# Kernel tuning notes

Measured on AMD Instinct MI355X. Metric: run time of the kernel, lower is better.

## Reference

```python
import jax, jax.numpy as jnp
import numpy as np

N_NODES = 5000
N_EDGES = 100000
MUL = 64            # env_embed_multiplicity
LATENT = 256        # ScalarMLPFunction latent width
NODE_DIM = 64
RADIAL_DIM = 8
R_MAX = 5.0
P_CUT = 6.0
AVG_NEIGH = 20.0
W_ENV = MUL * 2     # env_weighter weight_numel: mul * n_input_irreps (0e, 1o)
INV_SQRT3 = 1.0 / np.sqrt(3.0)


def _w(k, fi, fo):
    return jax.random.normal(k, (fi, fo), dtype=jnp.float32) / np.sqrt(fi)


def setup_inputs() -> dict:
    key = jax.random.key(0)
    i = iter(jax.random.split(key, 24))
    inp = {}
    inp['node_attrs'] = jax.random.normal(next(i), (N_NODES, NODE_DIM), dtype=jnp.float32)
    inp['edge_radial_attrs'] = jax.random.uniform(next(i), (N_EDGES, RADIAL_DIM), dtype=jnp.float32)
    inp['edge_angular_attrs'] = jax.random.normal(next(i), (N_EDGES, 4), dtype=jnp.float32)
    inp['edge_lengths'] = jax.random.uniform(next(i), (N_EDGES,), dtype=jnp.float32) * R_MAX
    inp['edge_index'] = jax.random.randint(next(i), (2, N_EDGES), 0, N_NODES, dtype=jnp.int32)
    # two-body latent MLP (layer 0): in = 2*node_dim + radial_dim
    inp['tb_w0'] = _w(next(i), 2 * NODE_DIM + RADIAL_DIM, LATENT)
    inp['tb_w1'] = _w(next(i), LATENT, LATENT)
    inp['tb_w2'] = _w(next(i), LATENT, LATENT)
    # latent MLP (layer 1): in = latent + mul * n_scalar_outs(=2)
    inp['lat1_w0'] = _w(next(i), LATENT + 2 * MUL, LATENT)
    inp['lat1_w1'] = _w(next(i), LATENT, LATENT)
    # env_embed MLPs: layer0 emits env weights + per-channel gate + feature-init weights
    inp['env0_w'] = _w(next(i), LATENT, 2 * W_ENV + MUL)
    inp['env1_w'] = _w(next(i), LATENT, W_ENV + MUL)
    # per-irrep env linears (0e block, 1o block)
    inp['envlin0'] = jax.random.normal(next(i), (2, MUL, MUL), dtype=jnp.float32) / np.sqrt(MUL)
    inp['envlin1'] = jax.random.normal(next(i), (2, MUL, MUL), dtype=jnp.float32) / np.sqrt(MUL)
    # post-TP irrep linears: layer0 maps 2 blocks -> 1 block per irrep type
    inp['lin0_sw'] = jax.random.normal(next(i), (2, MUL, MUL), dtype=jnp.float32) / np.sqrt(2 * MUL)
    inp['lin0_vw'] = jax.random.normal(next(i), (2, MUL, MUL), dtype=jnp.float32) / np.sqrt(2 * MUL)
    # last layer keeps full_out_irreps: 2 blocks -> 2 blocks per irrep type
    inp['lin1_sw'] = jax.random.normal(next(i), (2, 2, MUL, MUL), dtype=jnp.float32) / np.sqrt(2 * MUL)
    inp['lin1_vw'] = jax.random.normal(next(i), (2, 2, MUL, MUL), dtype=jnp.float32) / np.sqrt(2 * MUL)
    # final latent: in = latent + mul*2 -> mul*2 scalar gates
    inp['fin_w0'] = _w(next(i), LATENT + 2 * MUL, LATENT)
    inp['fin_w1'] = _w(next(i), LATENT, 2 * MUL)
    inp['res_p'] = jnp.zeros((2,), dtype=jnp.float32)
    return inp


def _poly_cutoff(r):
    x = r / R_MAX
    p = P_CUT
    out = (1.0 - ((p + 1.0) * (p + 2.0) / 2.0) * x ** p
           + p * (p + 2.0) * x ** (p + 1.0)
           - (p * (p + 1.0) / 2.0) * x ** (p + 2.0))
    return jnp.where(x < 1.0, out, 0.0)


def _mlp(x, ws):
    for j, w in enumerate(ws):
        x = x @ w
        if j < len(ws) - 1:
            x = jax.nn.silu(x)
    return x


def _env_weighter(sh, w):
    # sh [E,4] = (0e | 1o), w [E, MUL*2] -> scalar [E,MUL], vector [E,MUL,3]
    w = w.reshape(-1, MUL, 2)
    return w[..., 0] * sh[:, None, 0], w[..., 1:2] * sh[:, None, 1:4]


def _tp_uuu(s1, v1, s2, v2):
    # per-channel (uuu) CG tensor product, instructions:
    #   0e x 0e -> 0e ; 1o x 1o -> 0e ; 0e x 1o -> 1o ; 1o x 0e -> 1o
    ts = jnp.stack([s1 * s2, jnp.sum(v1 * v2, -1) * INV_SQRT3], axis=1)          # [E,2,MUL]
    tv = jnp.stack([s1[..., None] * v2 * INV_SQRT3,
                    v1 * s2[..., None] * INV_SQRT3], axis=1)                      # [E,2,MUL,3]
    return ts, tv


def reference(node_attrs, edge_radial_attrs, edge_angular_attrs, edge_lengths,
              edge_index, tb_w0, tb_w1, tb_w2, lat1_w0, lat1_w1, env0_w, env1_w,
              envlin0, envlin1, lin0_sw, lin0_vw, lin1_sw, lin1_vw,
              fin_w0, fin_w1, res_p):
    center, neigh = edge_index[0], edge_index[1]
    cut = _poly_cutoff(edge_lengths)[:, None]                                     # [E,1]

    # ---- layer 0: two-body latent ----
    x = jnp.concatenate([node_attrs[center], node_attrs[neigh], edge_radial_attrs], -1)
    latents = cut * _mlp(x, [tb_w0, tb_w1, tb_w2])                                # [E,LATENT]

    w_all = latents @ env0_w
    w_env, gate, w_feat = (w_all[:, :W_ENV], w_all[:, W_ENV:W_ENV + MUL],
                           w_all[:, W_ENV + MUL:])
    fs, fv = _env_weighter(edge_angular_attrs, w_feat)                            # [E,MUL],[E,MUL,3]
    fs = fs * gate
    fv = fv * gate[..., None]
    es, ev = _env_weighter(edge_angular_attrs, w_env)
    ns = jax.ops.segment_sum(es, center, num_segments=N_NODES) / AVG_NEIGH        # [N,MUL]
    nv = jax.ops.segment_sum(ev, center, num_segments=N_NODES) / AVG_NEIGH        # [N,MUL,3]
    ns = jnp.einsum('nu,uv->nv', ns, envlin0[0])
    nv = jnp.einsum('nuc,uv->nvc', nv, envlin0[1])
    ts, tv = _tp_uuu(fs, fv, ns[center], nv[center])
    scalars = ts.reshape(-1, 2 * MUL)
    fs = jnp.einsum('eiu,iuv->ev', ts, lin0_sw)                                   # [E,MUL]
    fv = jnp.einsum('eiuc,iuv->evc', tv, lin0_vw)                                 # [E,MUL,3]

    # ---- layer 1: latent resnet + tp ----
    new_lat = _mlp(jnp.concatenate([latents, scalars], -1), [lat1_w0, lat1_w1])
    a = jax.nn.sigmoid(res_p[1])
    latents = jnp.sqrt(1.0 - a) * latents + jnp.sqrt(a) * cut * new_lat

    w_all = latents @ env1_w
    w_env, gate = w_all[:, :W_ENV], w_all[:, W_ENV:]
    fs = fs * gate
    fv = fv * gate[..., None]
    es, ev = _env_weighter(edge_angular_attrs, w_env)
    ns = jax.ops.segment_sum(es, center, num_segments=N_NODES) / AVG_NEIGH
    nv = jax.ops.segment_sum(ev, center, num_segments=N_NODES) / AVG_NEIGH
    ns = jnp.einsum('nu,uv->nv', ns, envlin1[0])
    nv = jnp.einsum('nuc,uv->nvc', nv, envlin1[1])
    ts, tv = _tp_uuu(fs, fv, ns[center], nv[center])
    scalars = ts.reshape(-1, 2 * MUL)
    fs = jnp.einsum('eiu,iouv->eov', ts, lin1_sw)                                 # [E,2,MUL]
    fv = jnp.einsum('eiuc,iouv->eovc', tv, lin1_vw)                               # [E,2,MUL,3]

    # ---- final latent gates the scalar channels, reshape back ----
    fin = _mlp(jnp.concatenate([latents, scalars], -1), [fin_w0, fin_w1])         # [E,2*MUL]
    fs = fs * fin.reshape(-1, 2, MUL)
    return jnp.concatenate([fs.reshape(-1, 2 * MUL), fv.reshape(-1, 2 * MUL * 3)], -1)  # [E,512]
```

## Files before the change

### kernel.cpp

```cpp
#include <hip/hip_runtime.h>
#include <math.h>

typedef unsigned short u16;
typedef unsigned int   u32;

#define E_EDGES 100000
#define NNODES  5000
#define INV_SQRT3 0.57735026918962576f
#define INV_AVG   0.05f

typedef short bf16x8 __attribute__((ext_vector_type(8)));
typedef float f32x4  __attribute__((ext_vector_type(4)));

__device__ __forceinline__ float us2f(u16 u) {
    union { float f; u32 i; } c; c.i = ((u32)u) << 16; return c.f;
}
__device__ __forceinline__ u16 f2us(float f) {
    union { float f; u32 i; } c; c.f = f;
    u32 x = c.i;
    x += 0x7fffu + ((x >> 16) & 1u);
    return (u16)(x >> 16);
}
__device__ __forceinline__ float siluf(float x) { return x / (1.f + expf(-x)); }

__device__ __forceinline__ void gl_lds16(const void* g, void* l) {
    auto* s = (const __attribute__((address_space(1))) void*)g;
    auto* d = (__attribute__((address_space(3))) void*)l;
    __builtin_amdgcn_global_load_lds(s, d, 16, 0, 0);
}

template <int EPI>
__global__ __launch_bounds__(256) void mgemm2_k(
    const u16* __restrict__ X1, int ldx1, int K1,
    const u16* __restrict__ X2, int ldx2, int K2,
    const u16* __restrict__ Wh, const u16* __restrict__ Wl, int ldk,
    u16* __restrict__ Y, int ldy, int M, int N,
    const float* __restrict__ cut, const float* __restrict__ resp,
    const u16* __restrict__ F, float* __restrict__ OUTF)
{
    __shared__ short lA[4096];
    __shared__ short lBh[4096];
    __shared__ short lBl[4096];
    const int lane = threadIdx.x & 63;
    const int w    = threadIdx.x >> 6;
    const int q    = lane >> 4;
    const int r16  = lane & 15;
    const int m0 = blockIdx.x * 128;
    const int n0 = blockIdx.y * 128;
    const int wr0 = (w >> 1) * 64;
    const int wc0 = (w & 1) * 64;
    const int Kt = K1 + K2;

    f32x4 acc[4][4];
#pragma unroll
    for (int i = 0; i < 4; ++i)
#pragma unroll
        for (int j = 0; j < 4; ++j) acc[i][j] = (f32x4){0.f, 0.f, 0.f, 0.f};

    for (int k0 = 0; k0 < Kt; k0 += 32) {
        const u16* xs; int ldx, kb;
        if (k0 < K1) { xs = X1; ldx = ldx1; kb = k0; }
        else         { xs = X2; ldx = ldx2; kb = k0 - K1; }
#pragma unroll
        for (int i = 0; i < 2; ++i) {
            const int j = w * 2 + i;
            int row = m0 + (j & 1) * 64 + lane;
            row = row < M ? row : M - 1;
            gl_lds16(xs + (size_t)row * ldx + kb + (j >> 1) * 8, &lA[j * 512]);
        }
#pragma unroll
        for (int i = 0; i < 2; ++i) {
            const int j = w * 2 + i;
            const size_t wo = (size_t)(n0 + (j & 1) * 64 + lane) * ldk + k0 + (j >> 1) * 8;
            gl_lds16(Wh + wo, &lBh[j * 512]);
            gl_lds16(Wl + wo, &lBl[j * 512]);
        }
        __syncthreads();
        bf16x8 a[4], bh[4], bl[4];
#pragma unroll
        for (int rt = 0; rt < 4; ++rt)
            a[rt] = *(const bf16x8*)&lA[q * 1024 + (wr0 + rt * 16 + r16) * 8];
#pragma unroll
        for (int ct = 0; ct < 4; ++ct) {
            bh[ct] = *(const bf16x8*)&lBh[q * 1024 + (wc0 + ct * 16 + r16) * 8];
            bl[ct] = *(const bf16x8*)&lBl[q * 1024 + (wc0 + ct * 16 + r16) * 8];
        }
#pragma unroll
        for (int rt = 0; rt < 4; ++rt)
#pragma unroll
            for (int ct = 0; ct < 4; ++ct) {
                acc[rt][ct] = __builtin_amdgcn_mfma_f32_16x16x32_bf16(a[rt], bh[ct], acc[rt][ct], 0, 0, 0);
                acc[rt][ct] = __builtin_amdgcn_mfma_f32_16x16x32_bf16(a[rt], bl[ct], acc[rt][ct], 0, 0, 0);
            }
        __syncthreads();
    }
    float c1 = 0.f, c2a = 0.f;
    if (EPI == 3) {
        float aa = 1.f / (1.f + expf(-resp[1]));
        c1 = sqrtf(1.f - aa);
        c2a = sqrtf(aa);
    }
#pragma unroll
    for (int rt = 0; rt < 4; ++rt) {
#pragma unroll
        for (int r = 0; r < 4; ++r) {
            const int row = m0 + wr0 + rt * 16 + q * 4 + r;
            if (row < M) {
                float sc = 1.f;
                if (EPI == 2) sc = cut[row];
                float c2 = 0.f;
                if (EPI == 3) c2 = c2a * cut[row];
                int e3 = 0, cc = 0;
                if (EPI == 5) { e3 = row / 3; cc = row - e3 * 3; }
#pragma unroll
                for (int ct = 0; ct < 4; ++ct) {
                    const int col = n0 + wc0 + ct * 16 + r16;
                    if (col < N) {
                        float v = acc[rt][ct][r];
                        if (EPI == 1) v = siluf(v);
                        if (EPI == 2) v *= sc;
                        if (EPI == 3) v = c1 * us2f(Y[(size_t)row * ldy + col]) + c2 * v;
                        if (EPI == 4) {
                            OUTF[(size_t)row * 512 + col] = v * us2f(F[(size_t)row * 128 + col]);
                        } else if (EPI == 5) {
                            OUTF[(size_t)e3 * 512 + 128 + (col >> 6) * 192 + (col & 63) * 3 + cc] = v;
                        } else {
                            Y[(size_t)row * ldy + col] = f2us(v);
                        }
                    }
                }
            }
        }
    }
}

__global__ __launch_bounds__(128) void mgemm_k(
    const u16* __restrict__ X1, int ldx1, int K1,
    const u16* __restrict__ Wh, const u16* __restrict__ Wl, int ldk,
    u16* __restrict__ Y, int ldy, int M)
{
    __shared__ short lA[4096];
    __shared__ short lBh[2048];
    __shared__ short lBl[2048];
    const int lane = threadIdx.x & 63;
    const int w    = threadIdx.x >> 6;
    const int q    = lane >> 4;
    const int r16  = lane & 15;
    const int m0 = blockIdx.x * 128;
    const int n0 = blockIdx.y * 64;
    const int Kt = K1;

    f32x4 acc[4][4];
#pragma unroll
    for (int i = 0; i < 4; ++i)
#pragma unroll
        for (int j = 0; j < 4; ++j) acc[i][j] = (f32x4){0.f, 0.f, 0.f, 0.f};

    for (int k0 = 0; k0 < Kt; k0 += 32) {
#pragma unroll
        for (int i = 0; i < 4; ++i) {
            const int j = w * 4 + i;
            int row = m0 + (j & 1) * 64 + lane;
            row = row < M ? row : M - 1;
            gl_lds16(X1 + (size_t)row * ldx1 + k0 + (j >> 1) * 8, &lA[j * 512]);
        }
#pragma unroll
        for (int i = 0; i < 2; ++i) {
            const int j = w * 2 + i;
            const size_t wo = (size_t)(n0 + lane) * ldk + k0 + j * 8;
            gl_lds16(Wh + wo, &lBh[j * 512]);
            gl_lds16(Wl + wo, &lBl[j * 512]);
        }
        __syncthreads();
        bf16x8 a[4], bh[4], bl[4];
#pragma unroll
        for (int rt = 0; rt < 4; ++rt)
            a[rt] = *(const bf16x8*)&lA[q * 1024 + (w * 64 + rt * 16 + r16) * 8];
#pragma unroll
        for (int ct = 0; ct < 4; ++ct) {
            bh[ct] = *(const bf16x8*)&lBh[q * 512 + (ct * 16 + r16) * 8];
            bl[ct] = *(const bf16x8*)&lBl[q * 512 + (ct * 16 + r16) * 8];
        }
#pragma unroll
        for (int rt = 0; rt < 4; ++rt)
#pragma unroll
            for (int ct = 0; ct < 4; ++ct) {
                acc[rt][ct] = __builtin_amdgcn_mfma_f32_16x16x32_bf16(a[rt], bh[ct], acc[rt][ct], 0, 0, 0);
                acc[rt][ct] = __builtin_amdgcn_mfma_f32_16x16x32_bf16(a[rt], bl[ct], acc[rt][ct], 0, 0, 0);
            }
        __syncthreads();
    }
#pragma unroll
    for (int rt = 0; rt < 4; ++rt) {
#pragma unroll
        for (int r = 0; r < 4; ++r) {
            const int row = m0 + w * 64 + rt * 16 + q * 4 + r;
            if (row < M) {
#pragma unroll
                for (int ct = 0; ct < 4; ++ct)
                    Y[(size_t)row * ldy + n0 + ct * 16 + r16] = f2us(acc[rt][ct][r]);
            }
        }
    }
}

template <int MODE>
__global__ __launch_bounds__(256) void split_w_k(
    const float* __restrict__ src, u16* __restrict__ hi, u16* __restrict__ lo,
    int Ksrc, int Nsrc, int Kpad, int Npad)
{
    int idx = blockIdx.x * 256 + threadIdx.x;
    if (idx >= Npad * Kpad) return;
    int n = idx / Kpad, k = idx - n * Kpad;
    float wv = 0.f;
    if (k < Ksrc && n < Nsrc) {
        if (MODE == 0) wv = src[(size_t)k * Nsrc + n];
        else           wv = src[(k >> 6) * 8192 + (n >> 6) * 4096 + (k & 63) * 64 + (n & 63)];
    }
    u16 h = f2us(wv);
    hi[idx] = h;
    lo[idx] = f2us(wv - us2f(h));
}

__global__ __launch_bounds__(256) void prep_edges_k(
    const float* __restrict__ na, const float* __restrict__ radial,
    const float* __restrict__ lengths, const int* __restrict__ eidx,
    u16* __restrict__ X0, float* __restrict__ cut)
{
    int idx = blockIdx.x * 256 + threadIdx.x;
    if (idx >= E_EDGES * 160) return;
    int e = idx / 160;
    int k = idx - e * 160;
    float v = 0.f;
    if (k < 64)       v = na[(size_t)eidx[e] * 64 + k];
    else if (k < 128) v = na[(size_t)eidx[E_EDGES + e] * 64 + (k - 64)];
    else if (k < 136) v = radial[(size_t)e * 8 + (k - 128)];
    X0[idx] = f2us(v);
    if (k == 136) {
        float x = lengths[e] * 0.2f;
        float x3 = x * x * x;
        float x6 = x3 * x3, x7 = x6 * x, x8 = x7 * x;
        float o = 1.f - 28.f * x6 + 48.f * x7 - 21.f * x8;
        cut[e] = (x < 1.f) ? o : 0.f;
    }
}

__global__ __launch_bounds__(256) void hist_k(const int* __restrict__ eidx, int* __restrict__ cnt)
{
    int e = blockIdx.x * 256 + threadIdx.x;
    if (e < E_EDGES) atomicAdd(&cnt[eidx[e]], 1);
}

__global__ __launch_bounds__(256) void scan_k(const int* __restrict__ cnt, int* __restrict__ offs)
{
    __shared__ int buf[256];
    __shared__ int base;
    if (threadIdx.x == 0) base = 0;
    __syncthreads();
    for (int start = 0; start < NNODES; start += 256) {
        int i = start + threadIdx.x;
        int v = (i < NNODES) ? cnt[i] : 0;
        buf[threadIdx.x] = v;
        __syncthreads();
        for (int d = 1; d < 256; d <<= 1) {
            int t = (threadIdx.x >= d) ? buf[threadIdx.x - d] : 0;
            __syncthreads();
            buf[threadIdx.x] += t;
            __syncthreads();
        }
        if (i < NNODES) offs[i] = base + buf[threadIdx.x] - v;
        __syncthreads();
        if (threadIdx.x == 255) base += buf[255];
        __syncthreads();
    }
}

__global__ __launch_bounds__(256) void scatter_k(
    const int* __restrict__ eidx, const int* __restrict__ offs,
    int* __restrict__ cur, int* __restrict__ perm)
{
    int e = blockIdx.x * 256 + threadIdx.x;
    if (e >= E_EDGES) return;
    int n = eidx[e];
    int p = atomicAdd(&cur[n], 1);
    perm[offs[n] + p] = e;
}

template <int LD>
__global__ __launch_bounds__(64) void envsum_k(
    const u16* __restrict__ wall, const float* __restrict__ ang,
    const int* __restrict__ perm, const int* __restrict__ offs, const int* __restrict__ cnt,
    const float* __restrict__ envlin,
    float* __restrict__ ns_e, float* __restrict__ nv_e)
{
    const int n = blockIdx.x, lane = threadIdx.x;
    const int s = offs[n], c = cnt[n];
    float a0 = 0.f, a1 = 0.f, a2 = 0.f, a3 = 0.f;
    for (int i = 0; i < c; ++i) {
        int e = perm[s + i];
        u32 pw = *(const u32*)(wall + (size_t)e * LD + 2 * lane);
        float we0 = us2f((u16)(pw & 0xffffu)), we1 = us2f((u16)(pw >> 16));
        float4 sh = *(const float4*)(ang + (size_t)e * 4);
        a0 = fmaf(we0, sh.x, a0);
        a1 = fmaf(we1, sh.y, a1);
        a2 = fmaf(we1, sh.z, a2);
        a3 = fmaf(we1, sh.w, a3);
    }
    __shared__ float ss[64], sv0[64], sv1[64], sv2[64];
    ss[lane] = a0; sv0[lane] = a1; sv1[lane] = a2; sv2[lane] = a3;
    __syncthreads();
    const float* L0 = envlin;
    const float* L1 = envlin + 4096;
    float b0 = 0.f, b1 = 0.f, b2 = 0.f, b3 = 0.f;
#pragma unroll 8
    for (int u = 0; u < 64; ++u) {
        float l0 = L0[u * 64 + lane], l1 = L1[u * 64 + lane];
        b0 = fmaf(ss[u],  l0, b0);
        b1 = fmaf(sv0[u], l1, b1);
        b2 = fmaf(sv1[u], l1, b2);
        b3 = fmaf(sv2[u], l1, b3);
    }
    ns_e[n * 64 + lane]           = b0 * INV_AVG;
    nv_e[n * 192 + lane]          = b1 * INV_AVG;
    nv_e[n * 192 + 64 + lane]     = b2 * INV_AVG;
    nv_e[n * 192 + 128 + lane]    = b3 * INV_AVG;
}

__global__ __launch_bounds__(256) void tp0f_k(
    const u16* __restrict__ wall, const float* __restrict__ ang,
    const float* __restrict__ ns_e, const float* __restrict__ nv_e,
    const int* __restrict__ eidx, u16* __restrict__ ts, u16* __restrict__ tv)
{
    int idx = blockIdx.x * 256 + threadIdx.x;
    if (idx >= E_EDGES * 64) return;
    int e = idx >> 6, u = idx & 63;
    int ce = eidx[e];
    const u16* wr = wall + (size_t)e * 320;
    float g   = us2f(wr[128 + u]);
    u32 pw = *(const u32*)&wr[192 + 2 * u];
    float wf0 = us2f((u16)(pw & 0xffffu)), wf1 = us2f((u16)(pw >> 16));
    float4 sh = *(const float4*)(ang + (size_t)e * 4);
    float f  = wf0 * sh.x * g;
    float b0 = wf1 * sh.y * g;
    float b1 = wf1 * sh.z * g;
    float b2 = wf1 * sh.w * g;
    float ns = ns_e[ce * 64 + u];
    float n0 = nv_e[ce * 192 + u], n1 = nv_e[ce * 192 + 64 + u], n2 = nv_e[ce * 192 + 128 + u];
    ts[(size_t)e * 128 + u]      = f2us(f * ns);
    ts[(size_t)e * 128 + 64 + u] = f2us((b0 * n0 + b1 * n1 + b2 * n2) * INV_SQRT3);
    size_t tb = (size_t)e * 384;
    tv[tb + u]             = f2us(f * n0 * INV_SQRT3);
    tv[tb + 128 + u]       = f2us(f * n1 * INV_SQRT3);
    tv[tb + 256 + u]       = f2us(f * n2 * INV_SQRT3);
    tv[tb + 64 + u]        = f2us(b0 * ns * INV_SQRT3);
    tv[tb + 128 + 64 + u]  = f2us(b1 * ns * INV_SQRT3);
    tv[tb + 256 + 64 + u]  = f2us(b2 * ns * INV_SQRT3);
}

__global__ __launch_bounds__(256) void tp1f_k(
    const u16* __restrict__ fs1, const u16* __restrict__ fv1,
    const u16* __restrict__ wall,
    const float* __restrict__ ns_e, const float* __restrict__ nv_e,
    const int* __restrict__ eidx, u16* __restrict__ ts, u16* __restrict__ tv)
{
    int idx = blockIdx.x * 256 + threadIdx.x;
    if (idx >= E_EDGES * 64) return;
    int e = idx >> 6, u = idx & 63;
    int ce = eidx[e];
    float g = us2f(wall[(size_t)e * 192 + 128 + u]);
    float f  = us2f(fs1[(size_t)e * 64 + u]) * g;
    float b0 = us2f(fv1[((size_t)e * 3 + 0) * 64 + u]) * g;
    float b1 = us2f(fv1[((size_t)e * 3 + 1) * 64 + u]) * g;
    float b2 = us2f(fv1[((size_t)e * 3 + 2) * 64 + u]) * g;
    float ns = ns_e[ce * 64 + u];
    float n0 = nv_e[ce * 192 + u], n1 = nv_e[ce * 192 + 64 + u], n2 = nv_e[ce * 192 + 128 + u];
    ts[(size_t)e * 128 + u]      = f2us(f * ns);
    ts[(size_t)e * 128 + 64 + u] = f2us((b0 * n0 + b1 * n1 + b2 * n2) * INV_SQRT3);
    size_t tb = (size_t)e * 384;
    tv[tb + u]             = f2us(f * n0 * INV_SQRT3);
    tv[tb + 128 + u]       = f2us(f * n1 * INV_SQRT3);
    tv[tb + 256 + u]       = f2us(f * n2 * INV_SQRT3);
    tv[tb + 64 + u]        = f2us(b0 * ns * INV_SQRT3);
    tv[tb + 128 + 64 + u]  = f2us(b1 * ns * INV_SQRT3);
    tv[tb + 256 + 64 + u]  = f2us(b2 * ns * INV_SQRT3);
}

static void mgemm2(hipStream_t s, int epi,
                   const u16* X1, int ldx1, int K1,
                   const u16* X2, int ldx2, int K2,
                   const u16* Wh, const u16* Wl, int ldk,
                   u16* Y, int ldy, int M, int N,
                   const float* cut, const float* resp,
                   const u16* F, float* OUTF)
{
    dim3 grid((M + 127) / 128, (N + 127) / 128);
    dim3 block(256);
    if (epi == 0)      mgemm2_k<0><<<grid, block, 0, s>>>(X1, ldx1, K1, X2, ldx2, K2, Wh, Wl, ldk, Y, ldy, M, N, cut, resp, F, OUTF);
    else if (epi == 1) mgemm2_k<1><<<grid, block, 0, s>>>(X1, ldx1, K1, X2, ldx2, K2, Wh, Wl, ldk, Y, ldy, M, N, cut, resp, F, OUTF);
    else if (epi == 2) mgemm2_k<2><<<grid, block, 0, s>>>(X1, ldx1, K1, X2, ldx2, K2, Wh, Wl, ldk, Y, ldy, M, N, cut, resp, F, OUTF);
    else if (epi == 3) mgemm2_k<3><<<grid, block, 0, s>>>(X1, ldx1, K1, X2, ldx2, K2, Wh, Wl, ldk, Y, ldy, M, N, cut, resp, F, OUTF);
    else if (epi == 4) mgemm2_k<4><<<grid, block, 0, s>>>(X1, ldx1, K1, X2, ldx2, K2, Wh, Wl, ldk, Y, ldy, M, N, cut, resp, F, OUTF);
    else               mgemm2_k<5><<<grid, block, 0, s>>>(X1, ldx1, K1, X2, ldx2, K2, Wh, Wl, ldk, Y, ldy, M, N, cut, resp, F, OUTF);
}

static void split_w(hipStream_t s, int mode, const float* src, u16* hi, u16* lo,
                    int Ksrc, int Nsrc, int Kpad, int Npad)
{
    int n = Npad * Kpad;
    dim3 grid((n + 255) / 256), block(256);
    if (mode == 0) split_w_k<0><<<grid, block, 0, s>>>(src, hi, lo, Ksrc, Nsrc, Kpad, Npad);
    else           split_w_k<1><<<grid, block, 0, s>>>(src, hi, lo, Ksrc, Nsrc, Kpad, Npad);
}

extern "C" void kernel_launch(void* const* d_in, const int* in_sizes, int n_in,
                              void* d_out, int out_size, void* d_ws, size_t ws_size,
                              hipStream_t stream)
{
    const float* node_attrs = (const float*)d_in[0];
    const float* radial     = (const float*)d_in[1];
    const float* ang        = (const float*)d_in[2];
    const float* lengths    = (const float*)d_in[3];
    const int*   eidx       = (const int*)d_in[4];
    const float* tb_w0      = (const float*)d_in[5];
    const float* tb_w1      = (const float*)d_in[6];
    const float* tb_w2      = (const float*)d_in[7];
    const float* lat1_w0    = (const float*)d_in[8];
    const float* lat1_w1    = (const float*)d_in[9];
    const float* env0_w     = (const float*)d_in[10];
    const float* env1_w     = (const float*)d_in[11];
    const float* envlin0    = (const float*)d_in[12];
    const float* envlin1    = (const float*)d_in[13];
    const float* lin0_sw    = (const float*)d_in[14];
    const float* lin0_vw    = (const float*)d_in[15];
    const float* lin1_sw    = (const float*)d_in[16];
    const float* lin1_vw    = (const float*)d_in[17];
    const float* fin_w0     = (const float*)d_in[18];
    const float* fin_w1     = (const float*)d_in[19];
    const float* res_p      = (const float*)d_in[20];

    const size_t E = E_EDGES;
    unsigned char* ws = (unsigned char*)d_ws;
    size_t off = 0;
    auto take = [&](size_t n) -> void* {
        void* p = ws + off;
        off += (n + 255) & ~(size_t)255;
        return p;
    };
    u16*  X0   = (u16*)take(E * 160 * 2);
    float* cut = (float*)take(E * 4);
    u16*  hA   = (u16*)take(E * 256 * 2);
    u16*  hB   = (u16*)take(E * 256 * 2);
    u16*  lat  = (u16*)take(E * 256 * 2);
    u16*  wall = (u16*)take(E * 320 * 2);
    u16*  ts   = (u16*)take(E * 128 * 2);
    u16*  tv   = (u16*)take(E * 384 * 2);
    u16*  fs1  = (u16*)take(E * 64 * 2);
    u16*  fv1  = (u16*)take(E * 192 * 2);
    float* ns_e  = (float*)take((size_t)NNODES * 64 * 4);
    float* nv_e  = (float*)take((size_t)NNODES * 192 * 4);
    float* ns2_e = (float*)take((size_t)NNODES * 64 * 4);
    float* nv2_e = (float*)take((size_t)NNODES * 192 * 4);

    int* cnt  = (int*)take(NNODES * 4);
    int* cur  = (int*)take(NNODES * 4);
    int* offs = (int*)take(NNODES * 4);
    int* perm = (int*)take(E * 4);

    u16* W0h  = (u16*)take(256 * 160 * 2); u16* W0l  = (u16*)take(256 * 160 * 2);
    u16* W1h  = (u16*)take(65536 * 2);     u16* W1l  = (u16*)take(65536 * 2);
    u16* W2h  = (u16*)take(65536 * 2);     u16* W2l  = (u16*)take(65536 * 2);
    u16* We0h = (u16*)take(384 * 256 * 2); u16* We0l = (u16*)take(384 * 256 * 2);
    u16* WL0h = (u16*)take(98304 * 2);     u16* WL0l = (u16*)take(98304 * 2);
    u16* WL1h = (u16*)take(65536 * 2);     u16* WL1l = (u16*)take(65536 * 2);
    u16* We1h = (u16*)take(256 * 256 * 2); u16* We1l = (u16*)take(256 * 256 * 2);
    u16* S0h  = (u16*)take(8192 * 2);      u16* S0l  = (u16*)take(8192 * 2);
    u16* V0h  = (u16*)take(8192 * 2);      u16* V0l  = (u16*)take(8192 * 2);
    u16* S1h  = (u16*)take(16384 * 2);     u16* S1l  = (u16*)take(16384 * 2);
    u16* V1h  = (u16*)take(16384 * 2);     u16* V1l  = (u16*)take(16384 * 2);
    u16* WF0h = (u16*)take(98304 * 2);     u16* WF0l = (u16*)take(98304 * 2);
    u16* WF1h = (u16*)take(32768 * 2);     u16* WF1l = (u16*)take(32768 * 2);

    hipMemsetAsync(cnt, 0, NNODES * 4, stream);
    hipMemsetAsync(cur, 0, NNODES * 4, stream);

    split_w(stream, 0, tb_w0,   W0h,  W0l,  136, 256, 160, 256);
    split_w(stream, 0, tb_w1,   W1h,  W1l,  256, 256, 256, 256);
    split_w(stream, 0, tb_w2,   W2h,  W2l,  256, 256, 256, 256);
    split_w(stream, 0, env0_w,  We0h, We0l, 256, 320, 256, 384);
    split_w(stream, 0, lat1_w0, WL0h, WL0l, 384, 256, 384, 256);
    split_w(stream, 0, lat1_w1, WL1h, WL1l, 256, 256, 256, 256);
    split_w(stream, 0, env1_w,  We1h, We1l, 256, 192, 256, 256);
    split_w(stream, 0, lin0_sw, S0h,  S0l,  128, 64,  128, 64);
    split_w(stream, 0, lin0_vw, V0h,  V0l,  128, 64,  128, 64);
    split_w(stream, 1, lin1_sw, S1h,  S1l,  128, 128, 128, 128);
    split_w(stream, 1, lin1_vw, V1h,  V1l,  128, 128, 128, 128);
    split_w(stream, 0, fin_w0,  WF0h, WF0l, 384, 256, 384, 256);
    split_w(stream, 0, fin_w1,  WF1h, WF1l, 256, 128, 256, 128);

    prep_edges_k<<<(E_EDGES * 160) / 256, 256, 0, stream>>>(node_attrs, radial, lengths, eidx, X0, cut);

    hist_k<<<(E_EDGES + 255) / 256, 256, 0, stream>>>(eidx, cnt);
    scan_k<<<1, 256, 0, stream>>>(cnt, offs);
    scatter_k<<<(E_EDGES + 255) / 256, 256, 0, stream>>>(eidx, offs, cur, perm);

    mgemm2(stream, 1, X0, 160, 160, nullptr, 0, 0, W0h, W0l, 160, hA, 256, E_EDGES, 256, nullptr, nullptr, nullptr, nullptr);
    mgemm2(stream, 1, hA, 256, 256, nullptr, 0, 0, W1h, W1l, 256, hB, 256, E_EDGES, 256, nullptr, nullptr, nullptr, nullptr);
    mgemm2(stream, 2, hB, 256, 256, nullptr, 0, 0, W2h, W2l, 256, lat, 256, E_EDGES, 256, cut, nullptr, nullptr, nullptr);

    mgemm2(stream, 0, lat, 256, 256, nullptr, 0, 0, We0h, We0l, 256, wall, 320, E_EDGES, 320, nullptr, nullptr, nullptr, nullptr);
    envsum_k<320><<<NNODES, 64, 0, stream>>>(wall, ang, perm, offs, cnt, envlin0, ns_e, nv_e);
    tp0f_k<<<(E_EDGES * 64) / 256, 256, 0, stream>>>(wall, ang, ns_e, nv_e, eidx, ts, tv);
    {
        dim3 block(128);
        dim3 g1((E_EDGES + 127) / 128, 1);
        mgemm_k<<<g1, block, 0, stream>>>(ts, 128, 128, S0h, S0l, 128, fs1, 64, E_EDGES);
        dim3 g2((3 * E_EDGES + 127) / 128, 1);
        mgemm_k<<<g2, block, 0, stream>>>(tv, 128, 128, V0h, V0l, 128, fv1, 64, 3 * E_EDGES);
    }

    mgemm2(stream, 1, lat, 256, 256, ts, 128, 128, WL0h, WL0l, 384, hA, 256, E_EDGES, 256, nullptr, nullptr, nullptr, nullptr);
    mgemm2(stream, 3, hA, 256, 256, nullptr, 0, 0, WL1h, WL1l, 256, lat, 256, E_EDGES, 256, cut, res_p, nullptr, nullptr);

    mgemm2(stream, 0, lat, 256, 256, nullptr, 0, 0, We1h, We1l, 256, wall, 192, E_EDGES, 192, nullptr, nullptr, nullptr, nullptr);
    envsum_k<192><<<NNODES, 64, 0, stream>>>(wall, ang, perm, offs, cnt, envlin1, ns2_e, nv2_e);
    tp1f_k<<<(E_EDGES * 64) / 256, 256, 0, stream>>>(fs1, fv1, wall, ns2_e, nv2_e, eidx, ts, tv);

    mgemm2(stream, 1, lat, 256, 256, ts, 128, 128, WF0h, WF0l, 384, hA, 256, E_EDGES, 256, nullptr, nullptr, nullptr, nullptr);
    mgemm2(stream, 0, hA, 256, 256, nullptr, 0, 0, WF1h, WF1l, 256, hB, 128, E_EDGES, 128, nullptr, nullptr, nullptr, nullptr);

    mgemm2(stream, 4, ts, 128, 128, nullptr, 0, 0, S1h, S1l, 128, nullptr, 0, E_EDGES, 128, nullptr, nullptr, hB, (float*)d_out);
    mgemm2(stream, 5, tv, 128, 128, nullptr, 0, 0, V1h, V1l, 128, nullptr, 0, 3 * E_EDGES, 128, nullptr, nullptr, nullptr, (float*)d_out);
}
```

Baseline: 1.311 ms.

## Double-buffer LDS tiles in both MFMA GEMM kernels to overlap loads with compute

Both GEMM kernels now keep two LDS buffers for the A, B-high and B-low tiles. The next K-slice is issued with global_load_lds into the spare buffer before the MFMAs run on the current one, and a single barrier per iteration replaces the old load-barrier-compute-barrier sequence. The aim is to hide global-to-LDS latency behind matrix math. In exchange, LDS use per block doubles, to 48KB in the 256-thread kernel, which can lower the number of resident blocks per CU.

```diff
diff --git a/kernel.cpp b/kernel.cpp
--- a/kernel.cpp
+++ b/kernel.cpp
@@ -38,9 +38,9 @@
     const float* __restrict__ cut, const float* __restrict__ resp,
     const u16* __restrict__ F, float* __restrict__ OUTF)
 {
-    __shared__ short lA[4096];
-    __shared__ short lBh[4096];
-    __shared__ short lBl[4096];
+    __shared__ short lA[2][4096];
+    __shared__ short lBh[2][4096];
+    __shared__ short lBl[2][4096];
     const int lane = threadIdx.x & 63;
     const int w    = threadIdx.x >> 6;
     const int q    = lane >> 4;
@@ -51,13 +51,7 @@
     const int wc0 = (w & 1) * 64;
     const int Kt = K1 + K2;
 
-    f32x4 acc[4][4];
-#pragma unroll
-    for (int i = 0; i < 4; ++i)
-#pragma unroll
-        for (int j = 0; j < 4; ++j) acc[i][j] = (f32x4){0.f, 0.f, 0.f, 0.f};
-
-    for (int k0 = 0; k0 < Kt; k0 += 32) {
+    auto stage = [&](int k0, int buf) {
         const u16* xs; int ldx, kb;
         if (k0 < K1) { xs = X1; ldx = ldx1; kb = k0; }
         else         { xs = X2; ldx = ldx2; kb = k0 - K1; }
@@ -66,24 +60,36 @@
             const int j = w * 2 + i;
             int row = m0 + (j & 1) * 64 + lane;
             row = row < M ? row : M - 1;
-            gl_lds16(xs + (size_t)row * ldx + kb + (j >> 1) * 8, &lA[j * 512]);
+            gl_lds16(xs + (size_t)row * ldx + kb + (j >> 1) * 8, &lA[buf][j * 512]);
         }
 #pragma unroll
         for (int i = 0; i < 2; ++i) {
             const int j = w * 2 + i;
             const size_t wo = (size_t)(n0 + (j & 1) * 64 + lane) * ldk + k0 + (j >> 1) * 8;
-            gl_lds16(Wh + wo, &lBh[j * 512]);
-            gl_lds16(Wl + wo, &lBl[j * 512]);
-        }
-        __syncthreads();
+            gl_lds16(Wh + wo, &lBh[buf][j * 512]);
+            gl_lds16(Wl + wo, &lBl[buf][j * 512]);
+        }
+    };
+
+    f32x4 acc[4][4];
+#pragma unroll
+    for (int i = 0; i < 4; ++i)
+#pragma unroll
+        for (int j = 0; j < 4; ++j) acc[i][j] = (f32x4){0.f, 0.f, 0.f, 0.f};
+
+    stage(0, 0);
+    __syncthreads();
+    int cur = 0;
+    for (int k0 = 0; k0 < Kt; k0 += 32) {
+        if (k0 + 32 < Kt) stage(k0 + 32, cur ^ 1);
         bf16x8 a[4], bh[4], bl[4];
 #pragma unroll
         for (int rt = 0; rt < 4; ++rt)
-            a[rt] = *(const bf16x8*)&lA[q * 1024 + (wr0 + rt * 16 + r16) * 8];
+            a[rt] = *(const bf16x8*)&lA[cur][q * 1024 + (wr0 + rt * 16 + r16) * 8];
 #pragma unroll
         for (int ct = 0; ct < 4; ++ct) {
-            bh[ct] = *(const bf16x8*)&lBh[q * 1024 + (wc0 + ct * 16 + r16) * 8];
-            bl[ct] = *(const bf16x8*)&lBl[q * 1024 + (wc0 + ct * 16 + r16) * 8];
+            bh[ct] = *(const bf16x8*)&lBh[cur][q * 1024 + (wc0 + ct * 16 + r16) * 8];
+            bl[ct] = *(const bf16x8*)&lBl[cur][q * 1024 + (wc0 + ct * 16 + r16) * 8];
         }
 #pragma unroll
         for (int rt = 0; rt < 4; ++rt)
@@ -93,6 +99,7 @@
                 acc[rt][ct] = __builtin_amdgcn_mfma_f32_16x16x32_bf16(a[rt], bl[ct], acc[rt][ct], 0, 0, 0);
             }
         __syncthreads();
+        cur ^= 1;
     }
     float c1 = 0.f, c2a = 0.f;
     if (EPI == 3) {
@@ -139,9 +146,9 @@
     const u16* __restrict__ Wh, const u16* __restrict__ Wl, int ldk,
     u16* __restrict__ Y, int ldy, int M)
 {
-    __shared__ short lA[4096];
-    __shared__ short lBh[2048];
-    __shared__ short lBl[2048];
+    __shared__ short lA[2][4096];
+    __shared__ short lBh[2][2048];
+    __shared__ short lBl[2][2048];
     const int lane = threadIdx.x & 63;
     const int w    = threadIdx.x >> 6;
     const int q    = lane >> 4;
@@ -150,36 +157,42 @@
     const int n0 = blockIdx.y * 64;
     const int Kt = K1;
 
-    f32x4 acc[4][4];
-#pragma unroll
-    for (int i = 0; i < 4; ++i)
-#pragma unroll
-        for (int j = 0; j < 4; ++j) acc[i][j] = (f32x4){0.f, 0.f, 0.f, 0.f};
-
-    for (int k0 = 0; k0 < Kt; k0 += 32) {
+    auto stage = [&](int k0, int buf) {
 #pragma unroll
         for (int i = 0; i < 4; ++i) {
             const int j = w * 4 + i;
             int row = m0 + (j & 1) * 64 + lane;
             row = row < M ? row : M - 1;
-            gl_lds16(X1 + (size_t)row * ldx1 + k0 + (j >> 1) * 8, &lA[j * 512]);
+            gl_lds16(X1 + (size_t)row * ldx1 + k0 + (j >> 1) * 8, &lA[buf][j * 512]);
         }
 #pragma unroll
         for (int i = 0; i < 2; ++i) {
             const int j = w * 2 + i;
             const size_t wo = (size_t)(n0 + lane) * ldk + k0 + j * 8;
-            gl_lds16(Wh + wo, &lBh[j * 512]);
-            gl_lds16(Wl + wo, &lBl[j * 512]);
-        }
-        __syncthreads();
+            gl_lds16(Wh + wo, &lBh[buf][j * 512]);
+            gl_lds16(Wl + wo, &lBl[buf][j * 512]);
+        }
+    };
+
+    f32x4 acc[4][4];
+#pragma unroll
+    for (int i = 0; i < 4; ++i)
+#pragma unroll
+        for (int j = 0; j < 4; ++j) acc[i][j] = (f32x4){0.f, 0.f, 0.f, 0.f};
+
+    stage(0, 0);
+    __syncthreads();
+    int cur = 0;
+    for (int k0 = 0; k0 < Kt; k0 += 32) {
+        if (k0 + 32 < Kt) stage(k0 + 32, cur ^ 1);
         bf16x8 a[4], bh[4], bl[4];
 #pragma unroll
         for (int rt = 0; rt < 4; ++rt)
-            a[rt] = *(const bf16x8*)&lA[q * 1024 + (w * 64 + rt * 16 + r16) * 8];
+            a[rt] = *(const bf16x8*)&lA[cur][q * 1024 + (w * 64 + rt * 16 + r16) * 8];
 #pragma unroll
         for (int ct = 0; ct < 4; ++ct) {
-            bh[ct] = *(const bf16x8*)&lBh[q * 512 + (ct * 16 + r16) * 8];
-            bl[ct] = *(const bf16x8*)&lBl[q * 512 + (ct * 16 + r16) * 8];
+            bh[ct] = *(const bf16x8*)&lBh[cur][q * 512 + (ct * 16 + r16) * 8];
+            bl[ct] = *(const bf16x8*)&lBl[cur][q * 512 + (ct * 16 + r16) * 8];
         }
 #pragma unroll
         for (int rt = 0; rt < 4; ++rt)
@@ -189,6 +202,7 @@
                 acc[rt][ct] = __builtin_amdgcn_mfma_f32_16x16x32_bf16(a[rt], bl[ct], acc[rt][ct], 0, 0, 0);
             }
         __syncthreads();
+        cur ^= 1;
     }
 #pragma unroll
     for (int rt = 0; rt < 4; ++rt) {
```

After: 1.304 ms. Within noise of the previous version (-0.5%).
